# Kernel tuning notes

Measured on AMD Instinct MI355X. Metric: run time of the kernel, lower is better.

The kernel has to match this reference:

```python
import jax, jax.numpy as jnp
import numpy as np

BITW = 1
BITA = 3
BATCH = 8192
IN_CH = 4096
N_UNITS = 4096


def _quantize(x, k):
    # DoReFa uniform quantizer with straight-through estimator (round -> identity grad)
    n = float(2 ** k - 1)
    return x + jax.lax.stop_gradient(jnp.round(x * n) / n - x)


def _cabs(x):
    # clip magnitude to [0, 1]
    return jnp.minimum(1.0, jnp.abs(x))


def quantize_active(x, bitA):
    if bitA == 32:
        return x
    return _quantize(x, bitA)


def quantize_weight(w, bitW):
    if bitW == 32:
        return w
    if bitW == 1:
        # binary weights scaled by mean |w| (E is treated as constant)
        E = jax.lax.stop_gradient(jnp.mean(jnp.abs(w)))
        y = w / E
        # sign with straight-through gradient
        return (y + jax.lax.stop_gradient(jnp.sign(y) - y)) * E
    t = jnp.tanh(w)
    t = t / jnp.max(jnp.abs(t)) * 0.5 + 0.5
    return 2.0 * _quantize(t, bitW) - 1.0


def setup_inputs() -> dict:
    key = jax.random.key(0)
    k1, k2 = jax.random.split(key)
    inputs = jax.random.normal(k1, (BATCH, IN_CH), dtype=jnp.float32)
    # truncated_normal(stddev=0.1) init approximated with normal * 0.1
    W = jax.random.normal(k2, (IN_CH, N_UNITS), dtype=jnp.float32) * 0.1
    b = jnp.zeros((N_UNITS,), dtype=jnp.float32)
    return {"inputs": inputs, "W": W, "b": b}


def reference(inputs, W, b):
    q_in = quantize_active(_cabs(inputs), BITA)   # [B, IN] in {0..1} grid of 2^bitA-1 levels
    q_W = quantize_weight(W, BITW)                # [IN, OUT] binary (+-E)
    out = jnp.matmul(q_in, q_W) + b               # [B, OUT]
    return out
```

## Files before the change

### kernel.cpp

```cpp
#include <hip/hip_runtime.h>


static constexpr int BATCH  = 8192;
static constexpr int IN_CH  = 4096;
static constexpr int NUNITS = 4096;
static constexpr int TPB    = 256;

typedef int v4i __attribute__((ext_vector_type(4)));

static constexpr size_t A8_OFF   = 0;
static constexpr size_t A8_BYTES = (size_t)BATCH * IN_CH;
static constexpr size_t BT_OFF   = A8_OFF + A8_BYTES;
static constexpr size_t BT_BYTES = (size_t)NUNITS * IN_CH;
static constexpr int    NPART    = 4096;
static constexpr size_t PART_OFF = BT_OFF + BT_BYTES;
static constexpr size_t SCALE_OFF= PART_OFF + NPART * sizeof(float);

__global__ __launch_bounds__(TPB) void k_scale(const float* __restrict__ partials,
                                               float* __restrict__ scale) {
    __shared__ float red[TPB];
    float s = 0.f;
    for (int i = threadIdx.x; i < NPART; i += TPB) s += partials[i];
    red[threadIdx.x] = s;
    __syncthreads();
    for (int off = TPB / 2; off > 0; off >>= 1) {
        if ((int)threadIdx.x < off) red[threadIdx.x] += red[threadIdx.x + off];
        __syncthreads();
    }
    if (threadIdx.x == 0) {
        float E = red[0] / (float)((size_t)IN_CH * NUNITS);
        *scale = E / 7.0f;
    }
}

__device__ __forceinline__ unsigned int q4(float4 v) {
    unsigned int b0 = (unsigned int)(int)rintf(fminf(1.0f, fabsf(v.x)) * 7.0f);
    unsigned int b1 = (unsigned int)(int)rintf(fminf(1.0f, fabsf(v.y)) * 7.0f);
    unsigned int b2 = (unsigned int)(int)rintf(fminf(1.0f, fabsf(v.z)) * 7.0f);
    unsigned int b3 = (unsigned int)(int)rintf(fminf(1.0f, fabsf(v.w)) * 7.0f);
    return b0 | (b1 << 8) | (b2 << 16) | (b3 << 24);
}

__global__ __launch_bounds__(TPB) void k_quant_a(const float4* __restrict__ x4,
                                                 uint4* __restrict__ a16) {
    const size_t t = (size_t)blockIdx.x * TPB + threadIdx.x;
    uint4 o;
    o.x = q4(x4[t * 4 + 0]);
    o.y = q4(x4[t * 4 + 1]);
    o.z = q4(x4[t * 4 + 2]);
    o.w = q4(x4[t * 4 + 3]);
    a16[t] = o;
}

__global__ __launch_bounds__(TPB) void k_signT(const float* __restrict__ W,
                                               char* __restrict__ bt,
                                               float* __restrict__ partials) {
    __shared__ char tile[64][68];
    __shared__ float red[TPB];
    const int bk = blockIdx.x & 63;
    const int bn = blockIdx.x >> 6;
    const int t  = threadIdx.x;
    const int c  = t & 63;
    const int r0 = t >> 6;
    float asum = 0.f;
#pragma unroll
    for (int i = 0; i < 16; ++i) {
        int r = i * 4 + r0;
        float w = W[(size_t)(bk * 64 + r) * NUNITS + bn * 64 + c];
        asum += fabsf(w);
        tile[c][r] = (w > 0.f) ? 1 : ((w < 0.f) ? -1 : 0);
    }
    __syncthreads();
    const int n  = t >> 2;
    const int kk = (t & 3) * 16;
    char o[16];
#pragma unroll
    for (int j = 0; j < 16; ++j) o[j] = tile[n][kk + j];
    *(uint4*)(bt + (size_t)(bn * 64 + n) * IN_CH + bk * 64 + kk) = *(const uint4*)o;

    red[t] = asum;
    __syncthreads();
    for (int off = TPB / 2; off > 0; off >>= 1) {
        if (t < off) red[t] += red[t + off];
        __syncthreads();
    }
    if (t == 0) partials[blockIdx.x] = red[0];
}

__device__ __forceinline__ void gload_lds16(const void* g, void* l) {
    __builtin_amdgcn_global_load_lds((const __attribute__((address_space(1))) void*)g,
                                     (__attribute__((address_space(3))) void*)l,
                                     16, 0, 0);
}

#define VMCNT2   asm volatile("s_waitcnt vmcnt(2)" ::: "memory")
#define VMCNT0   asm volatile("s_waitcnt vmcnt(0)" ::: "memory")
#define LGKM0    asm volatile("s_waitcnt lgkmcnt(0)" ::: "memory")
#define SCHEDB   __builtin_amdgcn_sched_barrier(0)
#define BARRIER  __builtin_amdgcn_s_barrier()
#define PRIO1    __builtin_amdgcn_s_setprio(1)
#define PRIO0    __builtin_amdgcn_s_setprio(0)

static constexpr int NT = IN_CH / 128;

__global__ __launch_bounds__(512, 2) void k_gemm(const char* __restrict__ A8,
                                                 const char* __restrict__ BT,
                                                 const float* __restrict__ scale_p,
                                                 const float* __restrict__ bias,
                                                 float* __restrict__ out) {
    __shared__ char As[2][32768];
    __shared__ char Bs[2][32768];

    const int t    = threadIdx.x;
    const int bid  = blockIdx.x;
    const int swzb = (bid & 7) * 64 + (bid >> 3);
    const int bRow = swzb >> 4;
    const int bCol = swzb & 15;
    const int lane = t & 63;
    const int wid  = t >> 6;
    const int wm   = wid >> 2;
    const int wn   = wid & 3;
    const int lr   = lane & 15;
    const int lk4  = lane >> 4;

    const size_t aBase = (size_t)(bRow * 256) * IN_CH;
    const size_t bBase = (size_t)(bCol * 256) * IN_CH;

    const int ceff0 = (lk4 * 16) ^ ((lr & 7) << 4);
    const int ceff1 = ceff0 ^ 64;

    const int srow  = t >> 3;
    const int scol  = ((t & 7) * 16) ^ ((srow & 7) << 4);
    const int sldso = t * 16;

    v4i acc[8][4] = {};
    v4i a0[4][2], a1[4][2], b01[2][2], b23[2][2];

#define STAGE(kt, q)                                                                  \
    do {                                                                              \
        const int _b = (kt) & 1;                                                      \
        if ((q) < 4)                                                                  \
            gload_lds16(A8 + aBase + (size_t)((q) * 64 + srow) * IN_CH + (kt) * 128 + scol, \
                        &As[_b][(q & 3) * 8192 + sldso]);                             \
        else                                                                          \
            gload_lds16(BT + bBase + (size_t)(((q) - 4) * 64 + srow) * IN_CH + (kt) * 128 + scol, \
                        &Bs[_b][((q) - 4) * 8192 + sldso]);                           \
    } while (0)

#define READ_A0(Ab)                                                    \
    _Pragma("unroll") for (int m = 0; m < 4; ++m) {                    \
        const int ra = (wm * 128 + m * 16 + lr) * 128;                 \
        a0[m][0] = *(const v4i*)((Ab) + ra + ceff0);                   \
        a0[m][1] = *(const v4i*)((Ab) + ra + ceff1);                   \
    }
#define READ_A1(Ab)                                                    \
    _Pragma("unroll") for (int m = 0; m < 4; ++m) {                    \
        const int ra = (wm * 128 + (m + 4) * 16 + lr) * 128;           \
        a1[m][0] = *(const v4i*)((Ab) + ra + ceff0);                   \
        a1[m][1] = *(const v4i*)((Ab) + ra + ceff1);                   \
    }
#define READ_B01(Bb)                                                   \
    _Pragma("unroll") for (int n = 0; n < 2; ++n) {                    \
        const int rb = (wn * 64 + n * 16 + lr) * 128;                  \
        b01[n][0] = *(const v4i*)((Bb) + rb + ceff0);                  \
        b01[n][1] = *(const v4i*)((Bb) + rb + ceff1);                  \
    }
#define READ_B23(Bb)                                                   \
    _Pragma("unroll") for (int n = 0; n < 2; ++n) {                    \
        const int rb = (wn * 64 + (n + 2) * 16 + lr) * 128;            \
        b23[n][0] = *(const v4i*)((Bb) + rb + ceff0);                  \
        b23[n][1] = *(const v4i*)((Bb) + rb + ceff1);                  \
    }
#define MFMA16(arr, brr, mo, no)                                                       \
    PRIO1;                                                                             \
    _Pragma("unroll") for (int m = 0; m < 4; ++m)                                      \
        _Pragma("unroll") for (int n = 0; n < 2; ++n)                                  \
            _Pragma("unroll") for (int s = 0; s < 2; ++s)                              \
                acc[(mo) + m][(no) + n] = __builtin_amdgcn_mfma_i32_16x16x64_i8(       \
                    arr[m][s], brr[n][s], acc[(mo) + m][(no) + n], 0, 0, 0);           \
    PRIO0

#pragma unroll
    for (int q = 0; q < 8; ++q) STAGE(0, q);
    STAGE(1, 0); STAGE(1, 1);
    VMCNT2; SCHEDB;
    BARRIER;

    for (int T = 0; T < NT; T += 2) {
        const char* Ab0 = As[0]; const char* Bb0 = Bs[0];
        const char* Ab1 = As[1]; const char* Bb1 = Bs[1];
        const bool more = (T + 2 < NT);

        READ_A0(Ab0); READ_B01(Bb0);
        STAGE(T + 1, 2); STAGE(T + 1, 3);
        SCHEDB; BARRIER; LGKM0; SCHEDB;
        MFMA16(a0, b01, 0, 0); SCHEDB; BARRIER;

        READ_B23(Bb0);
        STAGE(T + 1, 4); STAGE(T + 1, 5);
        SCHEDB; BARRIER; LGKM0; SCHEDB;
        MFMA16(a0, b23, 0, 2); SCHEDB; BARRIER;

        READ_A1(Ab0);
        STAGE(T + 1, 6); STAGE(T + 1, 7);
        SCHEDB; BARRIER; LGKM0; SCHEDB;
        MFMA16(a1, b01, 4, 0); SCHEDB; BARRIER;

        if (more) { STAGE(T + 2, 0); STAGE(T + 2, 1); VMCNT2; }
        else      { VMCNT0; }
        SCHEDB; BARRIER; SCHEDB;
        MFMA16(a1, b23, 4, 2); SCHEDB; BARRIER;

        READ_A0(Ab1); READ_B01(Bb1);
        if (more) { STAGE(T + 2, 2); STAGE(T + 2, 3); }
        SCHEDB; BARRIER; LGKM0; SCHEDB;
        MFMA16(a0, b01, 0, 0); SCHEDB; BARRIER;

        READ_B23(Bb1);
        if (more) { STAGE(T + 2, 4); STAGE(T + 2, 5); }
        SCHEDB; BARRIER; LGKM0; SCHEDB;
        MFMA16(a0, b23, 0, 2); SCHEDB; BARRIER;

        READ_A1(Ab1);
        if (more) { STAGE(T + 2, 6); STAGE(T + 2, 7); }
        SCHEDB; BARRIER; LGKM0; SCHEDB;
        MFMA16(a1, b01, 4, 0); SCHEDB; BARRIER;

        if (more) { STAGE(T + 3, 0); STAGE(T + 3, 1); VMCNT2; }
        SCHEDB; BARRIER; SCHEDB;
        MFMA16(a1, b23, 4, 2); SCHEDB; BARRIER;
    }

    const float scale = *scale_p;
    const int orow0 = bRow * 256 + wm * 128;
    const int ocol0 = bCol * 256 + wn * 64;
#pragma unroll
    for (int m = 0; m < 8; ++m) {
#pragma unroll
        for (int n = 0; n < 4; ++n) {
            const int col = ocol0 + n * 16 + lr;
            const float bb = bias[col];
            const int rbase = orow0 + m * 16 + lk4 * 4;
#pragma unroll
            for (int j = 0; j < 4; ++j)
                out[(size_t)(rbase + j) * NUNITS + col] = scale * (float)acc[m][n][j] + bb;
        }
    }
#undef STAGE
#undef READ_A0
#undef READ_A1
#undef READ_B01
#undef READ_B23
#undef MFMA16
}

extern "C" void kernel_launch(void* const* d_in, const int* in_sizes, int n_in,
                              void* d_out, int out_size, void* d_ws, size_t ws_size,
                              hipStream_t stream) {
    const float* x  = (const float*)d_in[0];
    const float* W  = (const float*)d_in[1];
    const float* b  = (const float*)d_in[2];
    float* out      = (float*)d_out;

    char*  ws       = (char*)d_ws;
    char*  A8       = ws + A8_OFF;
    char*  BT       = ws + BT_OFF;
    float* partials = (float*)(ws + PART_OFF);
    float* scale    = (float*)(ws + SCALE_OFF);

    k_signT<<<(IN_CH / 64) * (NUNITS / 64), TPB, 0, stream>>>(W, BT, partials);
    k_scale<<<1, TPB, 0, stream>>>(partials, scale);
    k_quant_a<<<(BATCH * (IN_CH / 16)) / TPB, TPB, 0, stream>>>((const float4*)x, (uint4*)A8);
    k_gemm<<<(BATCH / 256) * (NUNITS / 256), 512, 0, stream>>>(A8, BT, scale, b, out);
}
```

Before: 195.1 us.

## Switch int8 GEMM mainloop to triple-buffered 64-wide K tiles with single barrier

The int8 MFMA GEMM mainloop now uses 64-wide K tiles in one unified LDS buffer ring of three slots (A and B halves together), replacing the double-buffered 128-wide A/B scheme. Loads are issued two tiles ahead, and the wait drops to vmcnt(4). Each tile then needs a single barrier before all 32 MFMAs, instead of eight barrier-separated sub-phases per pair of tiles. The goal is to cut barrier and wait overhead while keeping global-to-LDS loads overlapped. The cost is less fine-grained interleaving of LDS reads with MFMAs and twice as many K iterations.

```diff
diff --git a/kernel.cpp b/kernel.cpp
--- a/kernel.cpp
+++ b/kernel.cpp
@@ -93,7 +93,7 @@
                                      16, 0, 0);
 }
 
-#define VMCNT2   asm volatile("s_waitcnt vmcnt(2)" ::: "memory")
+#define VMCNT4   asm volatile("s_waitcnt vmcnt(4)" ::: "memory")
 #define VMCNT0   asm volatile("s_waitcnt vmcnt(0)" ::: "memory")
 #define LGKM0    asm volatile("s_waitcnt lgkmcnt(0)" ::: "memory")
 #define SCHEDB   __builtin_amdgcn_sched_barrier(0)
@@ -101,15 +101,14 @@
 #define PRIO1    __builtin_amdgcn_s_setprio(1)
 #define PRIO0    __builtin_amdgcn_s_setprio(0)
 
-static constexpr int NT = IN_CH / 128;
+static constexpr int NT = IN_CH / 64;
 
 __global__ __launch_bounds__(512, 2) void k_gemm(const char* __restrict__ A8,
                                                  const char* __restrict__ BT,
                                                  const float* __restrict__ scale_p,
                                                  const float* __restrict__ bias,
                                                  float* __restrict__ out) {
-    __shared__ char As[2][32768];
-    __shared__ char Bs[2][32768];
+    __shared__ char Ms[3][32768];
 
     const int t    = threadIdx.x;
     const int bid  = blockIdx.x;
@@ -126,110 +125,54 @@
     const size_t aBase = (size_t)(bRow * 256) * IN_CH;
     const size_t bBase = (size_t)(bCol * 256) * IN_CH;
 
-    const int ceff0 = (lk4 * 16) ^ ((lr & 7) << 4);
-    const int ceff1 = ceff0 ^ 64;
+    const int aswz = ((lk4 ^ (lr & 7)) << 4);
+    const int bswz = aswz ^ 64;
 
     const int srow  = t >> 3;
-    const int scol  = ((t & 7) * 16) ^ ((srow & 7) << 4);
-    const int sldso = t * 16;
+    const int pslot = t & 7;
+    const int lslot = pslot ^ (srow & 7);
+    const char* mbase = (lslot < 4) ? (A8 + aBase) : (BT + bBase);
+    const char* sbase = mbase + (size_t)srow * IN_CH + (size_t)((lslot & 3) << 4);
 
     v4i acc[8][4] = {};
-    v4i a0[4][2], a1[4][2], b01[2][2], b23[2][2];
-
-#define STAGE(kt, q)                                                                  \
-    do {                                                                              \
-        const int _b = (kt) & 1;                                                      \
-        if ((q) < 4)                                                                  \
-            gload_lds16(A8 + aBase + (size_t)((q) * 64 + srow) * IN_CH + (kt) * 128 + scol, \
-                        &As[_b][(q & 3) * 8192 + sldso]);                             \
-        else                                                                          \
-            gload_lds16(BT + bBase + (size_t)(((q) - 4) * 64 + srow) * IN_CH + (kt) * 128 + scol, \
-                        &Bs[_b][((q) - 4) * 8192 + sldso]);                           \
+
+#define STAGE4(kt, STG)                                                         \
+    _Pragma("unroll") for (int h = 0; h < 4; ++h)                               \
+        gload_lds16(sbase + (size_t)h * 64 * IN_CH + (size_t)(kt) * 64,         \
+                    (STG) + h * 8192 + wid * 1024)
+
+#define TILE(kt, CUR, STG, LAST)                                                \
+    do {                                                                        \
+        SCHEDB; LGKM0;                                                         \
+        if (LAST) { VMCNT0; } else { VMCNT4; }                                  \
+        BARRIER; SCHEDB;                                                        \
+        if ((kt) + 2 < NT) { STAGE4((kt) + 2, STG); }                           \
+        v4i a_[8], b_[4];                                                       \
+        _Pragma("unroll") for (int m = 0; m < 8; ++m)                           \
+            a_[m] = *(const v4i*)((CUR) + (wm * 128 + m * 16 + lr) * 128 + aswz); \
+        _Pragma("unroll") for (int n = 0; n < 4; ++n)                           \
+            b_[n] = *(const v4i*)((CUR) + (wn * 64 + n * 16 + lr) * 128 + bswz); \
+        PRIO1;                                                                  \
+        _Pragma("unroll") for (int m = 0; m < 8; ++m)                           \
+            _Pragma("unroll") for (int n = 0; n < 4; ++n)                       \
+                acc[m][n] = __builtin_amdgcn_mfma_i32_16x16x64_i8(              \
+                    a_[m], b_[n], acc[m][n], 0, 0, 0);                          \
+        PRIO0;                                                                  \
     } while (0)
 
-#define READ_A0(Ab)                                                    \
-    _Pragma("unroll") for (int m = 0; m < 4; ++m) {                    \
-        const int ra = (wm * 128 + m * 16 + lr) * 128;                 \
-        a0[m][0] = *(const v4i*)((Ab) + ra + ceff0);                   \
-        a0[m][1] = *(const v4i*)((Ab) + ra + ceff1);                   \
-    }
-#define READ_A1(Ab)                                                    \
-    _Pragma("unroll") for (int m = 0; m < 4; ++m) {                    \
-        const int ra = (wm * 128 + (m + 4) * 16 + lr) * 128;           \
-        a1[m][0] = *(const v4i*)((Ab) + ra + ceff0);                   \
-        a1[m][1] = *(const v4i*)((Ab) + ra + ceff1);                   \
-    }
-#define READ_B01(Bb)                                                   \
-    _Pragma("unroll") for (int n = 0; n < 2; ++n) {                    \
-        const int rb = (wn * 64 + n * 16 + lr) * 128;                  \
-        b01[n][0] = *(const v4i*)((Bb) + rb + ceff0);                  \
-        b01[n][1] = *(const v4i*)((Bb) + rb + ceff1);                  \
-    }
-#define READ_B23(Bb)                                                   \
-    _Pragma("unroll") for (int n = 0; n < 2; ++n) {                    \
-        const int rb = (wn * 64 + (n + 2) * 16 + lr) * 128;            \
-        b23[n][0] = *(const v4i*)((Bb) + rb + ceff0);                  \
-        b23[n][1] = *(const v4i*)((Bb) + rb + ceff1);                  \
-    }
-#define MFMA16(arr, brr, mo, no)                                                       \
-    PRIO1;                                                                             \
-    _Pragma("unroll") for (int m = 0; m < 4; ++m)                                      \
-        _Pragma("unroll") for (int n = 0; n < 2; ++n)                                  \
-            _Pragma("unroll") for (int s = 0; s < 2; ++s)                              \
-                acc[(mo) + m][(no) + n] = __builtin_amdgcn_mfma_i32_16x16x64_i8(       \
-                    arr[m][s], brr[n][s], acc[(mo) + m][(no) + n], 0, 0, 0);           \
-    PRIO0
-
-#pragma unroll
-    for (int q = 0; q < 8; ++q) STAGE(0, q);
-    STAGE(1, 0); STAGE(1, 1);
-    VMCNT2; SCHEDB;
-    BARRIER;
-
-    for (int T = 0; T < NT; T += 2) {
-        const char* Ab0 = As[0]; const char* Bb0 = Bs[0];
-        const char* Ab1 = As[1]; const char* Bb1 = Bs[1];
-        const bool more = (T + 2 < NT);
-
-        READ_A0(Ab0); READ_B01(Bb0);
-        STAGE(T + 1, 2); STAGE(T + 1, 3);
-        SCHEDB; BARRIER; LGKM0; SCHEDB;
-        MFMA16(a0, b01, 0, 0); SCHEDB; BARRIER;
-
-        READ_B23(Bb0);
-        STAGE(T + 1, 4); STAGE(T + 1, 5);
-        SCHEDB; BARRIER; LGKM0; SCHEDB;
-        MFMA16(a0, b23, 0, 2); SCHEDB; BARRIER;
-
-        READ_A1(Ab0);
-        STAGE(T + 1, 6); STAGE(T + 1, 7);
-        SCHEDB; BARRIER; LGKM0; SCHEDB;
-        MFMA16(a1, b01, 4, 0); SCHEDB; BARRIER;
-
-        if (more) { STAGE(T + 2, 0); STAGE(T + 2, 1); VMCNT2; }
-        else      { VMCNT0; }
-        SCHEDB; BARRIER; SCHEDB;
-        MFMA16(a1, b23, 4, 2); SCHEDB; BARRIER;
-
-        READ_A0(Ab1); READ_B01(Bb1);
-        if (more) { STAGE(T + 2, 2); STAGE(T + 2, 3); }
-        SCHEDB; BARRIER; LGKM0; SCHEDB;
-        MFMA16(a0, b01, 0, 0); SCHEDB; BARRIER;
-
-        READ_B23(Bb1);
-        if (more) { STAGE(T + 2, 4); STAGE(T + 2, 5); }
-        SCHEDB; BARRIER; LGKM0; SCHEDB;
-        MFMA16(a0, b23, 0, 2); SCHEDB; BARRIER;
-
-        READ_A1(Ab1);
-        if (more) { STAGE(T + 2, 6); STAGE(T + 2, 7); }
-        SCHEDB; BARRIER; LGKM0; SCHEDB;
-        MFMA16(a1, b01, 4, 0); SCHEDB; BARRIER;
-
-        if (more) { STAGE(T + 3, 0); STAGE(T + 3, 1); VMCNT2; }
-        SCHEDB; BARRIER; SCHEDB;
-        MFMA16(a1, b23, 4, 2); SCHEDB; BARRIER;
-    }
+    char* B0 = (char*)Ms[0];
+    char* B1 = (char*)Ms[1];
+    char* B2 = (char*)Ms[2];
+
+    STAGE4(0, B0);
+    STAGE4(1, B1);
+
+    for (int T = 0; T < NT - 1; T += 3) {
+        TILE(T,     B0, B2, false);
+        TILE(T + 1, B1, B0, false);
+        TILE(T + 2, B2, B1, false);
+    }
+    TILE(NT - 1, B0, B2, true);
 
     const float scale = *scale_p;
     const int orow0 = bRow * 256 + wm * 128;
@@ -246,12 +189,8 @@
                 out[(size_t)(rbase + j) * NUNITS + col] = scale * (float)acc[m][n][j] + bb;
         }
     }
-#undef STAGE
-#undef READ_A0
-#undef READ_A1
-#undef READ_B01
-#undef READ_B23
-#undef MFMA16
+#undef STAGE4
+#undef TILE
 }
 
 extern "C" void kernel_launch(void* const* d_in, const int* in_sizes, int n_in,
```

Result: faster. 181.9 us (-6.8%).

## Restructure GEMM main loop: single-step iteration, batched staging, no sched barriers

Applied to the files above, without the earlier changes.

Replaces the manually unrolled two-tile loop with a single-tile loop that alternates LDS buffers. Global-to-LDS staging for the next tile is now issued in groups of four chunks at two points per iteration instead of two chunks at each of four points, with the vmcnt wait raised to match. All sched_barrier fences are removed so the compiler can interleave instructions freely. This aims to cut code size and scheduling constraints, but it changes how loads overlap with MFMA work and may alter instruction ordering and register pressure.

```diff
diff --git a/kernel.cpp b/kernel.cpp
--- a/kernel.cpp
+++ b/kernel.cpp
@@ -93,10 +93,9 @@
                                      16, 0, 0);
 }
 
-#define VMCNT2   asm volatile("s_waitcnt vmcnt(2)" ::: "memory")
+#define VMCNT4   asm volatile("s_waitcnt vmcnt(4)" ::: "memory")
 #define VMCNT0   asm volatile("s_waitcnt vmcnt(0)" ::: "memory")
 #define LGKM0    asm volatile("s_waitcnt lgkmcnt(0)" ::: "memory")
-#define SCHEDB   __builtin_amdgcn_sched_barrier(0)
 #define BARRIER  __builtin_amdgcn_s_barrier()
 #define PRIO1    __builtin_amdgcn_s_setprio(1)
 #define PRIO0    __builtin_amdgcn_s_setprio(0)
@@ -182,53 +181,35 @@
 
 #pragma unroll
     for (int q = 0; q < 8; ++q) STAGE(0, q);
-    STAGE(1, 0); STAGE(1, 1);
-    VMCNT2; SCHEDB;
+    STAGE(1, 0); STAGE(1, 1); STAGE(1, 2); STAGE(1, 3);
+    VMCNT4;
     BARRIER;
 
-    for (int T = 0; T < NT; T += 2) {
-        const char* Ab0 = As[0]; const char* Bb0 = Bs[0];
-        const char* Ab1 = As[1]; const char* Bb1 = Bs[1];
-        const bool more = (T + 2 < NT);
-
-        READ_A0(Ab0); READ_B01(Bb0);
-        STAGE(T + 1, 2); STAGE(T + 1, 3);
-        SCHEDB; BARRIER; LGKM0; SCHEDB;
-        MFMA16(a0, b01, 0, 0); SCHEDB; BARRIER;
-
-        READ_B23(Bb0);
-        STAGE(T + 1, 4); STAGE(T + 1, 5);
-        SCHEDB; BARRIER; LGKM0; SCHEDB;
-        MFMA16(a0, b23, 0, 2); SCHEDB; BARRIER;
-
-        READ_A1(Ab0);
-        STAGE(T + 1, 6); STAGE(T + 1, 7);
-        SCHEDB; BARRIER; LGKM0; SCHEDB;
-        MFMA16(a1, b01, 4, 0); SCHEDB; BARRIER;
-
-        if (more) { STAGE(T + 2, 0); STAGE(T + 2, 1); VMCNT2; }
-        else      { VMCNT0; }
-        SCHEDB; BARRIER; SCHEDB;
-        MFMA16(a1, b23, 4, 2); SCHEDB; BARRIER;
-
-        READ_A0(Ab1); READ_B01(Bb1);
-        if (more) { STAGE(T + 2, 2); STAGE(T + 2, 3); }
-        SCHEDB; BARRIER; LGKM0; SCHEDB;
-        MFMA16(a0, b01, 0, 0); SCHEDB; BARRIER;
-
-        READ_B23(Bb1);
-        if (more) { STAGE(T + 2, 4); STAGE(T + 2, 5); }
-        SCHEDB; BARRIER; LGKM0; SCHEDB;
-        MFMA16(a0, b23, 0, 2); SCHEDB; BARRIER;
-
-        READ_A1(Ab1);
-        if (more) { STAGE(T + 2, 6); STAGE(T + 2, 7); }
-        SCHEDB; BARRIER; LGKM0; SCHEDB;
-        MFMA16(a1, b01, 4, 0); SCHEDB; BARRIER;
-
-        if (more) { STAGE(T + 3, 0); STAGE(T + 3, 1); VMCNT2; }
-        SCHEDB; BARRIER; SCHEDB;
-        MFMA16(a1, b23, 4, 2); SCHEDB; BARRIER;
+    for (int T = 0; T < NT; ++T) {
+        const char* Ab = As[T & 1];
+        const char* Bb = Bs[T & 1];
+
+        READ_A0(Ab); READ_B01(Bb);
+        if (T + 1 < NT) { STAGE(T + 1, 4); STAGE(T + 1, 5); STAGE(T + 1, 6); STAGE(T + 1, 7); }
+        BARRIER; LGKM0;
+        MFMA16(a0, b01, 0, 0);
+        BARRIER;
+
+        READ_B23(Bb);
+        BARRIER; LGKM0;
+        MFMA16(a0, b23, 0, 2);
+        BARRIER;
+
+        READ_A1(Ab);
+        BARRIER; LGKM0;
+        MFMA16(a1, b01, 4, 0);
+        BARRIER;
+
+        if (T + 2 < NT) { STAGE(T + 2, 0); STAGE(T + 2, 1); STAGE(T + 2, 2); STAGE(T + 2, 3); }
+        if (T + 1 < NT) { VMCNT4; } else { VMCNT0; }
+        BARRIER;
+        MFMA16(a1, b23, 4, 2);
+        BARRIER;
     }
 
     const float scale = *scale_p;
```

Measured after the change: 196.2 us. About the same (+0.6%).
